# Kernel optimization log

Hardware: AMD Instinct MI355X
Metric: run time of the kernel (lower is better)

Reference implementation:

```python
import jax, jax.numpy as jnp
import numpy as np
import math

DIM = 1024
D_FF = 1024
B = 128


def setup_inputs() -> dict:
    key = jax.random.key(0)
    ks = jax.random.split(key, 13)
    s = 1.0 / math.sqrt(DIM)
    sf = 1.0 / math.sqrt(D_FF)
    return {
        "x": jax.random.normal(ks[0], (B, DIM), dtype=jnp.float32),
        "Wq": jax.random.uniform(ks[1], (DIM, DIM), jnp.float32, -s, s),
        "bq": jax.random.uniform(ks[2], (DIM,), jnp.float32, -s, s),
        "Wk": jax.random.uniform(ks[3], (DIM, DIM), jnp.float32, -s, s),
        "bk": jax.random.uniform(ks[4], (DIM,), jnp.float32, -s, s),
        "Wv": jax.random.uniform(ks[5], (DIM, DIM), jnp.float32, -s, s),
        "bv": jax.random.uniform(ks[6], (DIM,), jnp.float32, -s, s),
        "Wo": jax.random.uniform(ks[7], (DIM, DIM), jnp.float32, -s, s),
        "bo": jax.random.uniform(ks[8], (DIM,), jnp.float32, -s, s),
        "W1": jax.random.uniform(ks[9], (D_FF, DIM), jnp.float32, -s, s),
        "b1": jax.random.uniform(ks[10], (D_FF,), jnp.float32, -s, s),
        "W2": jax.random.uniform(ks[11], (DIM, D_FF), jnp.float32, -sf, sf),
        "b2": jax.random.uniform(ks[12], (DIM,), jnp.float32, -sf, sf),
    }


def reference(x, Wq, bq, Wk, bk, Wv, bv, Wo, bo, W1, b1, W2, b2):
    # Attention (eval mode: dropout is identity)
    q = x @ Wq.T + bq                      # [B, D]
    k = x @ Wk.T + bk                      # [B, D]
    v = x @ Wv.T + bv                      # [B, D]
    inv_sqrt_dk = 1.0 / math.sqrt(DIM)
    # per-sample outer product: weights[b, i, j] = q[b,i] * k[b,j] / sqrt(d_k)
    weights = (q[:, :, None] * k[:, None, :]) * inv_sqrt_dk  # [B, D, D]
    nw = jax.nn.softmax(weights, axis=-1)                    # [B, D, D]
    attn_out = jnp.einsum('bij,bj->bi', nw, v)               # [B, D]
    attn_out = attn_out @ Wo.T + bo
    # residual 1
    x2 = x + attn_out
    # FFN
    h = jax.nn.relu(x2 @ W1.T + b1)        # [B, d_ff]
    ff = h @ W2.T + b2                     # [B, D]
    out = x2 + ff
    return (out, nw)
```

## Files before the change

### kernel.cpp

```cpp
#include <hip/hip_runtime.h>

#define DIM   1024
#define BATCH 128
#define MAT   (BATCH*DIM)
#define NROWS MAT
#define DS    32

#define Q1W   10240
#define Q1    16384
#define A_WO  16384
#define B_WO  34816
#define A_W1  41984
#define B_W1  60416
#define A_W2  67584
#define B_W2  86016
#define MBASE 93184

struct Params {
  const float *x,*Wq,*bq,*Wk,*bk,*Wv,*bv,*Wo,*bo,*W1,*b1,*W2,*b2;
  float *out,*nw;
  float *q,*k,*v,*araw,*x2,*h,*P;
};

template<bool WRITE, bool AR>
__device__ __forceinline__ void attn_row(const Params& p, int row, int lane)
{
  const int b = row >> 10;
  const float c = p.q[row] * 0.03125f;
  const float4* __restrict__ k4 = (const float4*)(p.k + ((size_t)b<<10));
  const float4* __restrict__ v4 = (const float4*)(p.v + ((size_t)b<<10));
  float sum=0.f, dot=0.f;
  float4 e[4];
#pragma unroll
  for (int t=0;t<4;++t) {
    const float4 kk = k4[lane + 64*t];
    float4 pp;
    pp.x=__expf(c*kk.x); pp.y=__expf(c*kk.y);
    pp.z=__expf(c*kk.z); pp.w=__expf(c*kk.w);
    sum += (pp.x+pp.y)+(pp.z+pp.w);
    if (AR) {
      const float4 vv = v4[lane + 64*t];
      dot += pp.x*vv.x + pp.y*vv.y + pp.z*vv.z + pp.w*vv.w;
    }
    e[t]=pp;
  }
#pragma unroll
  for (int off=32; off>=1; off>>=1) {
    sum += __shfl_xor(sum, off);
    if (AR) dot += __shfl_xor(dot, off);
  }
  const float rinv = 1.f/sum;
  if (WRITE) {
    float4* o = (float4*)(p.nw + ((size_t)row<<10));
#pragma unroll
    for (int t=0;t<4;++t) {
      float4 pp=e[t];
      pp.x*=rinv; pp.y*=rinv; pp.z*=rinv; pp.w*=rinv;
      o[lane + 64*t] = pp;
    }
  }
  if (AR && lane==0) p.araw[row] = dot*rinv;
}

__device__ __forceinline__ void write_rows(const Params& p, int r0, int n, int lane)
{
#pragma unroll 1
  for (int r = r0; r < r0 + n; ++r) attn_row<true,false>(p, r, lane);
}

__device__ __forceinline__ void gemm_tile(
    const float* __restrict__ X, const float* __restrict__ W,
    float* __restrict__ Pout, int n0, int k0, int KC,
    float* xt, float* wt)
{
  const int tid = threadIdx.x;
  const int tn = tid & 15, tb = tid >> 4;
  const int b_base = tb*8, n_base = tn*4;
  float acc[8][4];
#pragma unroll
  for (int i=0;i<8;++i)
#pragma unroll
    for (int j=0;j<4;++j) acc[i][j]=0.f;

  for (int s=0; s<KC/DS; ++s) {
    const int kk = k0 + s*DS;
#pragma unroll
    for (int r=0;r<4;++r) {
      const int row = (tid>>3) + 32*r;
      const int c0  = (tid&7)*4;
      const float4 vv = *(const float4*)(X + (size_t)row*DIM + kk + c0);
      xt[(c0+0)*132+row]=vv.x; xt[(c0+1)*132+row]=vv.y;
      xt[(c0+2)*132+row]=vv.z; xt[(c0+3)*132+row]=vv.w;
    }
#pragma unroll
    for (int r=0;r<2;++r) {
      const int row = (tid>>3) + 32*r;
      const int c0  = (tid&7)*4;
      const float4 vv = *(const float4*)(W + (size_t)(n0+row)*DIM + kk + c0);
      wt[(c0+0)*68+row]=vv.x; wt[(c0+1)*68+row]=vv.y;
      wt[(c0+2)*68+row]=vv.z; wt[(c0+3)*68+row]=vv.w;
    }
    __syncthreads();
#pragma unroll 4
    for (int d=0; d<DS; ++d) {
      const float4 xa0 = *(const float4*)&xt[d*132 + b_base];
      const float4 xa1 = *(const float4*)&xt[d*132 + b_base + 4];
      const float4 wa  = *(const float4*)&wt[d*68  + n_base];
      const float xr[8] = {xa0.x,xa0.y,xa0.z,xa0.w, xa1.x,xa1.y,xa1.z,xa1.w};
      const float wr[4] = {wa.x,wa.y,wa.z,wa.w};
#pragma unroll
      for (int bb=0;bb<8;++bb)
#pragma unroll
        for (int nn=0;nn<4;++nn) acc[bb][nn] += xr[bb]*wr[nn];
    }
    __syncthreads();
  }
#pragma unroll
  for (int bb=0;bb<8;++bb) {
    const float4 st = make_float4(acc[bb][0],acc[bb][1],acc[bb][2],acc[bb][3]);
    *(float4*)(Pout + (size_t)(b_base+bb)*DIM + n0 + n_base) = st;
  }
}

__global__ __launch_bounds__(256) void qkv_partial(
    const float* __restrict__ X, const float* __restrict__ W0,
    const float* __restrict__ W1, const float* __restrict__ W2,
    float* __restrict__ P)
{
  __shared__ float xt[DS*132];
  __shared__ float wt[DS*68];
  const int z = blockIdx.z;
  const float* W = (z==0)?W0:(z==1)?W1:W2;
  gemm_tile(X, W, P + (size_t)(z*8+blockIdx.y)*MAT,
            blockIdx.x*64, blockIdx.y*128, 128, xt, wt);
}

__global__ __launch_bounds__(256) void qkv_reduce(Params p)
{
  const int t = blockIdx.x*256 + threadIdx.x;
  const int z = t >> 15, idx4 = t & 32767;
  const float4* Pz = (const float4*)(p.P + (size_t)z*8*MAT);
  const float*  bias = (z==0) ? p.bq : (z==1) ? p.bk : p.bv;
  float* outz = (z==0) ? p.q : (z==1) ? p.k : p.v;
  float4 s = Pz[idx4];
#pragma unroll
  for (int sp=1; sp<8; ++sp) {
    const float4 t2 = Pz[sp*(MAT/4)+idx4];
    s.x+=t2.x; s.y+=t2.y; s.z+=t2.z; s.w+=t2.w;
  }
  const float4 b4 = ((const float4*)bias)[idx4 & 255];
  s.x+=b4.x; s.y+=b4.y; s.z+=b4.z; s.w+=b4.w;
  ((float4*)outz)[idx4] = s;
}

__global__ __launch_bounds__(256,4) void attn_mixed(Params p)
{
  const int bid = blockIdx.x, tid = threadIdx.x;
  const int wave = tid>>6, lane = tid&63;
  if (bid < 768) {
    const int gw = bid*4 + wave;
    int r0 = gw*43, r1 = r0 + 43;
    if (r1 > NROWS) r1 = NROWS;
#pragma unroll 1
    for (int r = r0; r < r1; ++r) attn_row<false,true>(p, r, lane);
    write_rows(p, Q1W + gw*2, 2, lane);
  } else {
    const int gw2 = (bid-768)*4 + wave;
    write_rows(p, gw2*10, 10, lane);
  }
}

__global__ __launch_bounds__(256,4) void chainA(Params p,
    const float* __restrict__ X, const float* __restrict__ W, int wbase)
{
  __shared__ float xt[DS*132];
  __shared__ float wt[DS*68];
  const int bid = blockIdx.x, tid = threadIdx.x;
  const int wave = tid>>6, lane = tid&63;
  if (bid < 256) {
    gemm_tile(X, W, p.P + (size_t)(bid&15)*MAT, (bid>>4)*64, (bid&15)*64, 64, xt, wt);
  } else {
    const int gw = (bid-256)*4 + wave;
    write_rows(p, wbase + gw*6, 6, lane);
  }
}

__global__ __launch_bounds__(256,4) void chainB(Params p,
    const float* __restrict__ bias, const float* __restrict__ extra,
    float* __restrict__ out, int relu, int wbase)
{
  const int bid = blockIdx.x, tid = threadIdx.x;
  const int wave = tid>>6, lane = tid&63;
  if (bid < 128) {
    const int idx4 = bid*256 + tid;
    const float4* P4 = (const float4*)p.P;
    float4 s = P4[idx4];
#pragma unroll
    for (int sp=1; sp<16; ++sp) {
      const float4 t2 = P4[sp*(MAT/4)+idx4];
      s.x+=t2.x; s.y+=t2.y; s.z+=t2.z; s.w+=t2.w;
    }
    const float4 b4 = ((const float4*)bias)[idx4 & 255];
    s.x+=b4.x; s.y+=b4.y; s.z+=b4.z; s.w+=b4.w;
    if (relu) { s.x=fmaxf(s.x,0.f); s.y=fmaxf(s.y,0.f);
                s.z=fmaxf(s.z,0.f); s.w=fmaxf(s.w,0.f); }
    if (extra) {
      const float4 e = ((const float4*)extra)[idx4];
      s.x+=e.x; s.y+=e.y; s.z+=e.z; s.w+=e.w;
    }
    ((float4*)out)[idx4] = s;
  } else {
    const int gw = (bid-128)*4 + wave;
    write_rows(p, wbase + gw*2, 2, lane);
  }
}

__global__ __launch_bounds__(256,4) void mopup(Params p)
{
  const int gw = blockIdx.x*4 + (threadIdx.x>>6);
  const int lane = threadIdx.x & 63;
#pragma unroll 1
  for (int row = MBASE + gw; row < NROWS; row += 4096)
    attn_row<true,false>(p, row, lane);
}

extern "C" void kernel_launch(void* const* d_in, const int* in_sizes, int n_in,
                              void* d_out, int out_size, void* d_ws, size_t ws_size,
                              hipStream_t stream)
{
  (void)in_sizes; (void)n_in; (void)out_size; (void)ws_size;
  Params p;
  p.x  = (const float*)d_in[0];
  p.Wq = (const float*)d_in[1];  p.bq = (const float*)d_in[2];
  p.Wk = (const float*)d_in[3];  p.bk = (const float*)d_in[4];
  p.Wv = (const float*)d_in[5];  p.bv = (const float*)d_in[6];
  p.Wo = (const float*)d_in[7];  p.bo = (const float*)d_in[8];
  p.W1 = (const float*)d_in[9];  p.b1 = (const float*)d_in[10];
  p.W2 = (const float*)d_in[11]; p.b2 = (const float*)d_in[12];
  p.out = (float*)d_out;
  p.nw  = p.out + MAT;
  float* ws = (float*)d_ws;
  p.q    = ws;         p.k  = ws + MAT;   p.v = ws + 2*MAT;
  p.araw = ws + 3*MAT; p.x2 = ws + 4*MAT; p.h = ws + 5*MAT;
  p.P    = ws + 6*MAT;

  qkv_partial<<<dim3(16,8,3), 256, 0, stream>>>(p.x, p.Wq, p.Wk, p.Wv, p.P);
  qkv_reduce<<<384, 256, 0, stream>>>(p);

  attn_mixed<<<1024, 256, 0, stream>>>(p);

  chainA<<<1024, 256, 0, stream>>>(p, p.araw, p.Wo, A_WO);
  chainB<<<1024, 256, 0, stream>>>(p, p.bo, p.x, p.x2, 0, B_WO);

  chainA<<<1024, 256, 0, stream>>>(p, p.x2, p.W1, A_W1);
  chainB<<<1024, 256, 0, stream>>>(p, p.b1, nullptr, p.h, 1, B_W1);

  chainA<<<1024, 256, 0, stream>>>(p, p.h, p.W2, A_W2);
  chainB<<<1024, 256, 0, stream>>>(p, p.b2, p.x2, p.out, 0, B_W2);

  mopup<<<1024, 256, 0, stream>>>(p);
}
```

Measured before the change: 195.3 us.

## Cache K/V in registers across rows, use nontemporal stores, rebalance row split

Softmax row processing now loads k and v for a batch once per contiguous run of rows and keeps them in registers, instead of reloading them for every row. The 512 MB nw output is written with nontemporal stores and weight tiles are read with nontemporal loads, to reduce cache pollution. The row partition across the overlapped kernels is redistributed: attn_mixed writes more nw rows, and mopup gives each wave a contiguous chunk so the register caching applies. The aim is to cut redundant L2 traffic and make better use of write bandwidth, at the cost of extra register pressure.

Result: faster. 177.7 us (median of 2 runs) (-9.0%).

```diff
diff --git a/kernel.cpp b/kernel.cpp
--- a/kernel.cpp
+++ b/kernel.cpp
@@ -6,15 +6,16 @@
 #define NROWS MAT
 #define DS    32
 
-#define Q1W   10240
-#define Q1    16384
-#define A_WO  16384
-#define B_WO  34816
-#define A_W1  41984
-#define B_W1  60416
-#define A_W2  67584
-#define B_W2  86016
-#define MBASE 93184
+typedef float f4n __attribute__((ext_vector_type(4)));
+
+#define Q_AT  28672
+#define A_WO  28672
+#define B_WO  47104
+#define A_W1  54272
+#define B_W1  72704
+#define A_W2  79872
+#define B_W2  98304
+#define MBASE 105472
 
 struct Params {
   const float *x,*Wq,*bq,*Wk,*bk,*Wv,*bv,*Wo,*bo,*W1,*b1,*W2,*b2;
@@ -23,49 +24,59 @@
 };
 
 template<bool WRITE, bool AR>
-__device__ __forceinline__ void attn_row(const Params& p, int row, int lane)
-{
-  const int b = row >> 10;
-  const float c = p.q[row] * 0.03125f;
-  const float4* __restrict__ k4 = (const float4*)(p.k + ((size_t)b<<10));
-  const float4* __restrict__ v4 = (const float4*)(p.v + ((size_t)b<<10));
-  float sum=0.f, dot=0.f;
-  float4 e[4];
-#pragma unroll
-  for (int t=0;t<4;++t) {
-    const float4 kk = k4[lane + 64*t];
-    float4 pp;
-    pp.x=__expf(c*kk.x); pp.y=__expf(c*kk.y);
-    pp.z=__expf(c*kk.z); pp.w=__expf(c*kk.w);
-    sum += (pp.x+pp.y)+(pp.z+pp.w);
-    if (AR) {
-      const float4 vv = v4[lane + 64*t];
-      dot += pp.x*vv.x + pp.y*vv.y + pp.z*vv.z + pp.w*vv.w;
-    }
-    e[t]=pp;
-  }
-#pragma unroll
-  for (int off=32; off>=1; off>>=1) {
-    sum += __shfl_xor(sum, off);
-    if (AR) dot += __shfl_xor(dot, off);
-  }
-  const float rinv = 1.f/sum;
-  if (WRITE) {
-    float4* o = (float4*)(p.nw + ((size_t)row<<10));
+__device__ __forceinline__ void attn_range(const Params& p, int r0, int r1, int lane)
+{
+  int bcur = -1;
+  float4 kr[4], vr[4];
+#pragma unroll 1
+  for (int row = r0; row < r1; ++row) {
+    const int b = row >> 10;
+    if (b != bcur) {
+      bcur = b;
+      const float4* __restrict__ k4 = (const float4*)(p.k + ((size_t)b<<10));
+#pragma unroll
+      for (int t=0;t<4;++t) kr[t] = k4[lane + 64*t];
+      if (AR) {
+        const float4* __restrict__ v4 = (const float4*)(p.v + ((size_t)b<<10));
+#pragma unroll
+        for (int t=0;t<4;++t) vr[t] = v4[lane + 64*t];
+      }
+    }
+    const float c = p.q[row] * 0.03125f;
+    float sum=0.f, dot=0.f;
+    float4 e[4];
 #pragma unroll
     for (int t=0;t<4;++t) {
-      float4 pp=e[t];
-      pp.x*=rinv; pp.y*=rinv; pp.z*=rinv; pp.w*=rinv;
-      o[lane + 64*t] = pp;
-    }
-  }
-  if (AR && lane==0) p.araw[row] = dot*rinv;
-}
-
-__device__ __forceinline__ void write_rows(const Params& p, int r0, int n, int lane)
-{
-#pragma unroll 1
-  for (int r = r0; r < r0 + n; ++r) attn_row<true,false>(p, r, lane);
+      const float4 kk = kr[t];
+      float4 pp;
+      pp.x=__expf(c*kk.x); pp.y=__expf(c*kk.y);
+      pp.z=__expf(c*kk.z); pp.w=__expf(c*kk.w);
+      sum += (pp.x+pp.y)+(pp.z+pp.w);
+      if (AR) {
+        const float4 vv = vr[t];
+        dot += pp.x*vv.x + pp.y*vv.y + pp.z*vv.z + pp.w*vv.w;
+      }
+      e[t]=pp;
+    }
+#pragma unroll
+    for (int off=32; off>=1; off>>=1) {
+      sum += __shfl_xor(sum, off);
+      if (AR) dot += __shfl_xor(dot, off);
+    }
+    const float rinv = 1.f/sum;
+    if (WRITE) {
+      f4n* o = (f4n*)(p.nw + ((size_t)row<<10));
+#pragma unroll
+      for (int t=0;t<4;++t) {
+        const float4 pp=e[t];
+        f4n st;
+        st.x = pp.x*rinv; st.y = pp.y*rinv;
+        st.z = pp.z*rinv; st.w = pp.w*rinv;
+        __builtin_nontemporal_store(st, &o[lane + 64*t]);
+      }
+    }
+    if (AR && lane==0) p.araw[row] = dot*rinv;
+  }
 }
 
 __device__ __forceinline__ void gemm_tile(
@@ -96,7 +107,8 @@
     for (int r=0;r<2;++r) {
       const int row = (tid>>3) + 32*r;
       const int c0  = (tid&7)*4;
-      const float4 vv = *(const float4*)(W + (size_t)(n0+row)*DIM + kk + c0);
+      const f4n vv = __builtin_nontemporal_load(
+          (const f4n*)(W + (size_t)(n0+row)*DIM + kk + c0));
       wt[(c0+0)*68+row]=vv.x; wt[(c0+1)*68+row]=vv.y;
       wt[(c0+2)*68+row]=vv.z; wt[(c0+3)*68+row]=vv.w;
     }
@@ -161,12 +173,10 @@
     const int gw = bid*4 + wave;
     int r0 = gw*43, r1 = r0 + 43;
     if (r1 > NROWS) r1 = NROWS;
-#pragma unroll 1
-    for (int r = r0; r < r1; ++r) attn_row<false,true>(p, r, lane);
-    write_rows(p, Q1W + gw*2, 2, lane);
+    attn_range<false,true>(p, r0, r1, lane);
   } else {
     const int gw2 = (bid-768)*4 + wave;
-    write_rows(p, gw2*10, 10, lane);
+    attn_range<true,false>(p, gw2*28, gw2*28 + 28, lane);
   }
 }
 
@@ -181,7 +191,7 @@
     gemm_tile(X, W, p.P + (size_t)(bid&15)*MAT, (bid>>4)*64, (bid&15)*64, 64, xt, wt);
   } else {
     const int gw = (bid-256)*4 + wave;
-    write_rows(p, wbase + gw*6, 6, lane);
+    attn_range<true,false>(p, wbase + gw*6, wbase + gw*6 + 6, lane);
   }
 }
 
@@ -211,7 +221,7 @@
     ((float4*)out)[idx4] = s;
   } else {
     const int gw = (bid-128)*4 + wave;
-    write_rows(p, wbase + gw*2, 2, lane);
+    attn_range<true,false>(p, wbase + gw*2, wbase + gw*2 + 2, lane);
   }
 }
 
@@ -219,9 +229,10 @@
 {
   const int gw = blockIdx.x*4 + (threadIdx.x>>6);
   const int lane = threadIdx.x & 63;
-#pragma unroll 1
-  for (int row = MBASE + gw; row < NROWS; row += 4096)
-    attn_row<true,false>(p, row, lane);
+  int r0, n;
+  if (gw < 1024) { r0 = MBASE + gw*7;             n = 7; }
+  else           { r0 = MBASE + 7168 + (gw-1024)*6; n = 6; }
+  attn_range<true,false>(p, r0, r0 + n, lane);
 }
 
 extern "C" void kernel_launch(void* const* d_in, const int* in_sizes, int n_in,
```
